# Performance work log

Hardware: AMD Instinct MI355X
Metric: run time of the kernel (lower is better)

Reference implementation:

```python
import jax, jax.numpy as jnp
import numpy as np


def setup_inputs() -> dict:
    key = jax.random.key(0)
    k1, k2, k3 = jax.random.split(key, 3)
    Lq, Lkv, H, D = 2048, 2048, 16, 128
    return {
        "query": jax.random.normal(k1, (Lq, H, D), dtype=jnp.float32),
        "key": jax.random.normal(k2, (Lkv, H, D), dtype=jnp.float32),
        "value": jax.random.normal(k3, (Lkv, H, D), dtype=jnp.float32),
    }


def reference(query, key, value):
    # query: [Lq, H, D], key: [Lkv, H, D], value: [Lkv, H, Dv]
    # Original module performs chunked online-softmax attention; the math is
    # exactly scaled-dot-product softmax attention with scale 1/sqrt(k_features).
    d = query.shape[-1]
    q = query * (1.0 / jnp.sqrt(jnp.asarray(d, dtype=query.dtype)))
    scores = jnp.einsum('qhd,khd->qhk', q, key)          # [Lq, H, Lkv]
    weights = jax.nn.softmax(scores, axis=-1)            # numerically stable online softmax equivalent
    out = jnp.einsum('qhk,khf->qhf', weights, value)     # [Lq, H, Dv]
    return out
```

## Files before the change

kernel.cpp:

```cpp
#include <hip/hip_runtime.h>
#include <hip/hip_bf16.h>

typedef __bf16 bf16x8 __attribute__((ext_vector_type(8)));
typedef __bf16 bf16x4 __attribute__((ext_vector_type(4)));
typedef __bf16 bf16x2 __attribute__((ext_vector_type(2)));
typedef float  f32x16 __attribute__((ext_vector_type(16)));
typedef float  f32x4  __attribute__((ext_vector_type(4)));

#define HD     2048
#define DH     128
#define KVT    64
#define NCH    16
#define NSPLIT 2
#define NROWS  32768
#define VSTR   68

__global__ __launch_bounds__(512, 2)
void fmha_kern(const float* __restrict__ Qg, const float* __restrict__ Kg,
               const float* __restrict__ Vg, float* __restrict__ wsO,
               float* __restrict__ wsML)
{
    __shared__ __align__(16) __bf16 klds[2][KVT * 128];
    __shared__ __align__(16) __bf16 vtlds[2][DH * VSTR];

    const int tid  = threadIdx.x;
    const int lane = tid & 63;
    const int wrp  = tid >> 6;
    const int g    = lane >> 5;
    const int l31  = lane & 31;

    const int b    = blockIdx.x;
    const int grp  = b & 31;
    const int qblk = b >> 5;
    const int h    = grp >> 1;
    const int sp   = grp & 1;
    const int t0   = sp * NCH;

    const float qscale = 1.4426950408889634f * 0.08838834764831845f;
    const int q = qblk * 256 + wrp * 32 + l31;

    bf16x8 qf[8];
    {
        const float* qrow = Qg + (size_t)q * HD + h * DH;
        #pragma unroll
        for (int j = 0; j < 8; ++j) {
            f32x4 a = *(const f32x4*)(qrow + j * 16 + 8 * g);
            f32x4 c = *(const f32x4*)(qrow + j * 16 + 8 * g + 4);
            bf16x8 f;
            f[0] = (__bf16)(a[0] * qscale); f[1] = (__bf16)(a[1] * qscale);
            f[2] = (__bf16)(a[2] * qscale); f[3] = (__bf16)(a[3] * qscale);
            f[4] = (__bf16)(c[0] * qscale); f[5] = (__bf16)(c[1] * qscale);
            f[6] = (__bf16)(c[2] * qscale); f[7] = (__bf16)(c[3] * qscale);
            qf[j] = f;
        }
    }

    const int krow = tid >> 3, kc = tid & 7;
    const int kvp  = tid & 31, vdv0 = (tid >> 5) * 8;
    const float* kbase = Kg + (size_t)h * DH;
    const float* vbase = Vg + (size_t)h * DH;

    f32x4 kreg0, kreg1, kreg2, kreg3, vreg0, vreg1, vreg2, vreg3;

    auto stage_load = [&](int t) {
        const float* kp = kbase + (size_t)(t * KVT + krow) * HD + kc * 8;
        kreg0 = *(const f32x4*)(kp);
        kreg1 = *(const f32x4*)(kp + 4);
        kreg2 = *(const f32x4*)(kp + 64);
        kreg3 = *(const f32x4*)(kp + 68);
        const float* vp = vbase + (size_t)(t * KVT + 2 * kvp) * HD + vdv0;
        vreg0 = *(const f32x4*)(vp);
        vreg1 = *(const f32x4*)(vp + 4);
        vreg2 = *(const f32x4*)(vp + HD);
        vreg3 = *(const f32x4*)(vp + HD + 4);
    };

    auto stage_write = [&](int buf) {
        bf16x8 k0, k1;
        k0[0]=(__bf16)kreg0[0]; k0[1]=(__bf16)kreg0[1]; k0[2]=(__bf16)kreg0[2]; k0[3]=(__bf16)kreg0[3];
        k0[4]=(__bf16)kreg1[0]; k0[5]=(__bf16)kreg1[1]; k0[6]=(__bf16)kreg1[2]; k0[7]=(__bf16)kreg1[3];
        k1[0]=(__bf16)kreg2[0]; k1[1]=(__bf16)kreg2[1]; k1[2]=(__bf16)kreg2[2]; k1[3]=(__bf16)kreg2[3];
        k1[4]=(__bf16)kreg3[0]; k1[5]=(__bf16)kreg3[1]; k1[6]=(__bf16)kreg3[2]; k1[7]=(__bf16)kreg3[3];
        const int swz = (krow & 7) << 3;
        *(bf16x8*)&klds[buf][krow * 128 + ((kc * 8) ^ swz)]      = k0;
        *(bf16x8*)&klds[buf][krow * 128 + ((kc * 8 + 64) ^ swz)] = k1;
        #pragma unroll
        for (int e = 0; e < 8; ++e) {
            bf16x2 w;
            w[0] = (__bf16)((e < 4) ? vreg0[e & 3] : vreg1[e & 3]);
            w[1] = (__bf16)((e < 4) ? vreg2[e & 3] : vreg3[e & 3]);
            *(bf16x2*)&vtlds[buf][(vdv0 + e) * VSTR + 2 * kvp] = w;
        }
    };

    auto block_sync = []() {
        asm volatile("s_waitcnt lgkmcnt(0)" ::: "memory");
        __builtin_amdgcn_s_barrier();
    };

    float mrun = -1e30f, lrun = 0.0f;
    f32x16 o0, o1, o2, o3;
    #pragma unroll
    for (int r = 0; r < 16; ++r) { o0[r] = 0.f; o1[r] = 0.f; o2[r] = 0.f; o3[r] = 0.f; }

    stage_load(t0);
    stage_write(0);
    stage_load(t0 + 1);
    block_sync();

    const int kswz = (l31 & 7) << 3;

    #pragma unroll 2
    for (int tt = 0; tt < NCH; ++tt) {
        const int cur = tt & 1;

        f32x16 s0, s1;
        #pragma unroll
        for (int r = 0; r < 16; ++r) { s0[r] = 0.f; s1[r] = 0.f; }
        __builtin_amdgcn_s_setprio(1);
        #pragma unroll
        for (int j = 0; j < 8; ++j) {
            bf16x8 kf0 = *(const bf16x8*)&klds[cur][l31 * 128 + ((j * 16 + 8 * g) ^ kswz)];
            s0 = __builtin_amdgcn_mfma_f32_32x32x16_bf16(kf0, qf[j], s0, 0, 0, 0);
            bf16x8 kf1 = *(const bf16x8*)&klds[cur][(32 + l31) * 128 + ((j * 16 + 8 * g) ^ kswz)];
            s1 = __builtin_amdgcn_mfma_f32_32x32x16_bf16(kf1, qf[j], s1, 0, 0, 0);
        }
        __builtin_amdgcn_s_setprio(0);

        if (tt + 1 < NCH) stage_write(cur ^ 1);
        if (tt + 2 < NCH) stage_load(t0 + tt + 2);

        float m16[8];
        #pragma unroll
        for (int r = 0; r < 8; ++r)
            m16[r] = fmaxf(fmaxf(s0[r], s0[r + 8]), fmaxf(s1[r], s1[r + 8]));
        float tmax = fmaxf(fmaxf(fmaxf(m16[0], m16[4]), fmaxf(m16[1], m16[5])),
                           fmaxf(fmaxf(m16[2], m16[6]), fmaxf(m16[3], m16[7])));
        tmax = fmaxf(tmax, __shfl_xor(tmax, 32, 64));

        if (__any(tmax > mrun + 8.0f)) {
            const float mnew  = fmaxf(mrun, tmax);
            const float alpha = __builtin_amdgcn_exp2f(mrun - mnew);
            lrun *= alpha;
            #pragma unroll
            for (int r = 0; r < 16; ++r) { o0[r] *= alpha; o1[r] *= alpha; o2[r] *= alpha; o3[r] *= alpha; }
            mrun = mnew;
        }

        float p0[16], p1[16];
        #pragma unroll
        for (int r = 0; r < 16; ++r) {
            p0[r] = __builtin_amdgcn_exp2f(s0[r] - mrun);
            p1[r] = __builtin_amdgcn_exp2f(s1[r] - mrun);
        }
        float ps = 0.f;
        #pragma unroll
        for (int r = 0; r < 16; ++r) ps += p0[r] + p1[r];
        lrun += ps;

        bf16x8 pfa0, pfa1, pfb0, pfb1;
        #pragma unroll
        for (int e = 0; e < 8; ++e) {
            pfa0[e] = (__bf16)p0[e]; pfa1[e] = (__bf16)p0[8 + e];
            pfb0[e] = (__bf16)p1[e]; pfb1[e] = (__bf16)p1[8 + e];
        }

        __builtin_amdgcn_s_setprio(1);
        #pragma unroll
        for (int bb = 0; bb < 4; ++bb) {
            const __bf16* vb = &vtlds[cur][(bb * 32 + l31) * VSTR];
            f32x16& oo = (bb == 0) ? o0 : (bb == 1) ? o1 : (bb == 2) ? o2 : o3;
            bf16x8 va;
            bf16x4 a0, a1;
            a0 = *(const bf16x4*)(vb + 4 * g);
            a1 = *(const bf16x4*)(vb + 8 + 4 * g);
            va[0]=a0[0]; va[1]=a0[1]; va[2]=a0[2]; va[3]=a0[3];
            va[4]=a1[0]; va[5]=a1[1]; va[6]=a1[2]; va[7]=a1[3];
            oo = __builtin_amdgcn_mfma_f32_32x32x16_bf16(va, pfa0, oo, 0, 0, 0);
            a0 = *(const bf16x4*)(vb + 16 + 4 * g);
            a1 = *(const bf16x4*)(vb + 24 + 4 * g);
            va[0]=a0[0]; va[1]=a0[1]; va[2]=a0[2]; va[3]=a0[3];
            va[4]=a1[0]; va[5]=a1[1]; va[6]=a1[2]; va[7]=a1[3];
            oo = __builtin_amdgcn_mfma_f32_32x32x16_bf16(va, pfa1, oo, 0, 0, 0);
            a0 = *(const bf16x4*)(vb + 32 + 4 * g);
            a1 = *(const bf16x4*)(vb + 40 + 4 * g);
            va[0]=a0[0]; va[1]=a0[1]; va[2]=a0[2]; va[3]=a0[3];
            va[4]=a1[0]; va[5]=a1[1]; va[6]=a1[2]; va[7]=a1[3];
            oo = __builtin_amdgcn_mfma_f32_32x32x16_bf16(va, pfb0, oo, 0, 0, 0);
            a0 = *(const bf16x4*)(vb + 48 + 4 * g);
            a1 = *(const bf16x4*)(vb + 56 + 4 * g);
            va[0]=a0[0]; va[1]=a0[1]; va[2]=a0[2]; va[3]=a0[3];
            va[4]=a1[0]; va[5]=a1[1]; va[6]=a1[2]; va[7]=a1[3];
            oo = __builtin_amdgcn_mfma_f32_32x32x16_bf16(va, pfb1, oo, 0, 0, 0);
        }
        __builtin_amdgcn_s_setprio(0);

        if (tt + 1 < NCH) block_sync();
    }

    const float ltot  = lrun + __shfl_xor(lrun, 32, 64);
    const int   rowid = q * 16 + h;

    float* orow = wsO + ((size_t)sp * NROWS + rowid) * 128;
    #pragma unroll
    for (int bb = 0; bb < 4; ++bb) {
        const f32x16& oo = (bb == 0) ? o0 : (bb == 1) ? o1 : (bb == 2) ? o2 : o3;
        #pragma unroll
        for (int jj = 0; jj < 4; ++jj) {
            f32x4 v;
            v[0] = oo[4*jj+0]; v[1] = oo[4*jj+1]; v[2] = oo[4*jj+2]; v[3] = oo[4*jj+3];
            *(f32x4*)(orow + bb * 32 + 8 * jj + 4 * g) = v;
        }
    }
    if (lane < 32) {
        float* ml = wsML + ((size_t)sp * NROWS + rowid) * 2;
        ml[0] = mrun;
        ml[1] = ltot;
    }
}

__global__ __launch_bounds__(256, 4)
void fmha_combine(const float* __restrict__ wsO, const float* __restrict__ wsML,
                  float* __restrict__ Og)
{
    const int tid   = threadIdx.x;
    const int rowid = blockIdx.x * 8 + (tid >> 5);
    const int c     = (tid & 31) * 4;

    float m[NSPLIT], l[NSPLIT];
    float M = -1e30f;
    #pragma unroll
    for (int s = 0; s < NSPLIT; ++s) {
        const float* ml = wsML + ((size_t)s * NROWS + rowid) * 2;
        m[s] = ml[0];
        l[s] = ml[1];
        M = fmaxf(M, m[s]);
    }
    float L = 0.f, w[NSPLIT];
    #pragma unroll
    for (int s = 0; s < NSPLIT; ++s) {
        w[s] = __builtin_amdgcn_exp2f(m[s] - M);
        L += l[s] * w[s];
    }
    const float inv = 1.0f / L;

    f32x4 acc; acc[0] = 0.f; acc[1] = 0.f; acc[2] = 0.f; acc[3] = 0.f;
    #pragma unroll
    for (int s = 0; s < NSPLIT; ++s) {
        f32x4 v = *(const f32x4*)(wsO + ((size_t)s * NROWS + rowid) * 128 + c);
        acc[0] += v[0] * w[s]; acc[1] += v[1] * w[s];
        acc[2] += v[2] * w[s]; acc[3] += v[3] * w[s];
    }
    f32x4 r;
    r[0] = acc[0] * inv; r[1] = acc[1] * inv; r[2] = acc[2] * inv; r[3] = acc[3] * inv;
    *(f32x4*)(Og + (size_t)rowid * 128 + c) = r;
}

__global__ __launch_bounds__(256, 2)
void fmha_fb(const float* __restrict__ Qg, const float* __restrict__ Kg,
             const float* __restrict__ Vg, float* __restrict__ Og)
{
    __shared__ __align__(16) __bf16 klds[2][32 * 128];
    __shared__ __align__(16) __bf16 vtlds[2][DH * 36];

    const int tid  = threadIdx.x;
    const int lane = tid & 63;
    const int wrp  = tid >> 6;
    const int g    = lane >> 5;
    const int l31  = lane & 31;

    const int b    = blockIdx.x;
    const int h    = 2 * (b & 7) + ((b >> 3) >> 4);
    const int qblk = (b >> 3) & 15;

    const float qscale = 1.4426950408889634f * 0.08838834764831845f;
    const int q = qblk * 128 + wrp * 32 + l31;

    bf16x8 qf[8];
    {
        const float* qrow = Qg + (size_t)q * HD + h * DH;
        #pragma unroll
        for (int db = 0; db < 8; ++db) {
            f32x4 a = *(const f32x4*)(qrow + db * 16 + 8 * g);
            f32x4 c = *(const f32x4*)(qrow + db * 16 + 8 * g + 4);
            bf16x8 f;
            f[0] = (__bf16)(a[0] * qscale); f[1] = (__bf16)(a[1] * qscale);
            f[2] = (__bf16)(a[2] * qscale); f[3] = (__bf16)(a[3] * qscale);
            f[4] = (__bf16)(c[0] * qscale); f[5] = (__bf16)(c[1] * qscale);
            f[6] = (__bf16)(c[2] * qscale); f[7] = (__bf16)(c[3] * qscale);
            qf[db] = f;
        }
    }

    const int krow = tid >> 3, kc = tid & 7;
    const int vkv  = tid & 31, vdv0 = (tid >> 5) * 16;
    const float* kbase = Kg + (size_t)h * DH;
    const float* vbase = Vg + (size_t)h * DH;

    f32x4 kreg0, kreg1, kreg2, kreg3, vreg0, vreg1, vreg2, vreg3;

    auto stage_load = [&](int t) {
        const float* kp = kbase + (size_t)(t * 32 + krow) * HD + kc * 8;
        kreg0 = *(const f32x4*)(kp);
        kreg1 = *(const f32x4*)(kp + 4);
        kreg2 = *(const f32x4*)(kp + 64);
        kreg3 = *(const f32x4*)(kp + 68);
        const float* vp = vbase + (size_t)(t * 32 + vkv) * HD + vdv0;
        vreg0 = *(const f32x4*)(vp);
        vreg1 = *(const f32x4*)(vp + 4);
        vreg2 = *(const f32x4*)(vp + 8);
        vreg3 = *(const f32x4*)(vp + 12);
    };

    auto stage_write = [&](int buf) {
        bf16x8 k0, k1;
        k0[0]=(__bf16)kreg0[0]; k0[1]=(__bf16)kreg0[1]; k0[2]=(__bf16)kreg0[2]; k0[3]=(__bf16)kreg0[3];
        k0[4]=(__bf16)kreg1[0]; k0[5]=(__bf16)kreg1[1]; k0[6]=(__bf16)kreg1[2]; k0[7]=(__bf16)kreg1[3];
        k1[0]=(__bf16)kreg2[0]; k1[1]=(__bf16)kreg2[1]; k1[2]=(__bf16)kreg2[2]; k1[3]=(__bf16)kreg2[3];
        k1[4]=(__bf16)kreg3[0]; k1[5]=(__bf16)kreg3[1]; k1[6]=(__bf16)kreg3[2]; k1[7]=(__bf16)kreg3[3];
        const int swz = (krow & 7) << 3;
        *(bf16x8*)&klds[buf][krow * 128 + ((kc * 8) ^ swz)]      = k0;
        *(bf16x8*)&klds[buf][krow * 128 + ((kc * 8 + 64) ^ swz)] = k1;
        #pragma unroll
        for (int jj = 0; jj < 4; ++jj) {
            f32x4 vv = (jj == 0) ? vreg0 : (jj == 1) ? vreg1 : (jj == 2) ? vreg2 : vreg3;
            #pragma unroll
            for (int e = 0; e < 4; ++e)
                vtlds[buf][(vdv0 + jj * 4 + e) * 36 + vkv] = (__bf16)vv[e];
        }
    };

    float mrun = -1e30f, lrun = 0.0f;
    f32x16 o0, o1, o2, o3;
    #pragma unroll
    for (int r = 0; r < 16; ++r) { o0[r] = 0.f; o1[r] = 0.f; o2[r] = 0.f; o3[r] = 0.f; }

    stage_load(0);
    stage_write(0);

    for (int tt = 0; tt < 64; ++tt) {
        const int cur = tt & 1;
        if (tt + 1 < 64) stage_load(tt + 1);
        __syncthreads();

        f32x16 sa, sb;
        #pragma unroll
        for (int r = 0; r < 16; ++r) { sa[r] = 0.f; sb[r] = 0.f; }
        const int kswz = (l31 & 7) << 3;
        #pragma unroll
        for (int db = 0; db < 4; ++db) {
            bf16x8 kfa = *(const bf16x8*)&klds[cur][l31 * 128 + (((2*db)   * 16 + g * 8) ^ kswz)];
            sa = __builtin_amdgcn_mfma_f32_32x32x16_bf16(kfa, qf[2*db],   sa, 0, 0, 0);
            bf16x8 kfb = *(const bf16x8*)&klds[cur][l31 * 128 + (((2*db+1) * 16 + g * 8) ^ kswz)];
            sb = __builtin_amdgcn_mfma_f32_32x32x16_bf16(kfb, qf[2*db+1], sb, 0, 0, 0);
        }
        f32x16 s;
        #pragma unroll
        for (int r = 0; r < 16; ++r) s[r] = sa[r] + sb[r];

        float m8[8];
        #pragma unroll
        for (int r = 0; r < 8; ++r) m8[r] = fmaxf(s[r], s[r + 8]);
        float tmax = fmaxf(fmaxf(fmaxf(m8[0], m8[4]), fmaxf(m8[1], m8[5])),
                           fmaxf(fmaxf(m8[2], m8[6]), fmaxf(m8[3], m8[7])));
        tmax = fmaxf(tmax, __shfl_xor(tmax, 32, 64));

        if (__any(tmax > mrun + 8.0f)) {
            const float mnew  = fmaxf(mrun, tmax);
            const float alpha = __builtin_amdgcn_exp2f(mrun - mnew);
            lrun *= alpha;
            #pragma unroll
            for (int r = 0; r < 16; ++r) { o0[r] *= alpha; o1[r] *= alpha; o2[r] *= alpha; o3[r] *= alpha; }
            mrun = mnew;
        }

        float p[16];
        #pragma unroll
        for (int r = 0; r < 16; ++r) p[r] = __builtin_amdgcn_exp2f(s[r] - mrun);
        float ps0 = 0, ps1 = 0, ps2 = 0, ps3 = 0;
        #pragma unroll
        for (int r = 0; r < 4; ++r) { ps0 += p[r]; ps1 += p[r+4]; ps2 += p[r+8]; ps3 += p[r+12]; }
        lrun += ((ps0 + ps1) + (ps2 + ps3));

        bf16x8 pf0, pf1;
        #pragma unroll
        for (int e = 0; e < 8; ++e) { pf0[e] = (__bf16)p[e]; pf1[e] = (__bf16)p[8 + e]; }

        #pragma unroll
        for (int bb = 0; bb < 4; ++bb) {
            const __bf16* vb = &vtlds[cur][(bb * 32 + l31) * 36];
            bf16x4 a0 = *(const bf16x4*)(vb + 4 * g);
            bf16x4 a1 = *(const bf16x4*)(vb + 8 + 4 * g);
            bf16x8 va;
            va[0]=a0[0]; va[1]=a0[1]; va[2]=a0[2]; va[3]=a0[3];
            va[4]=a1[0]; va[5]=a1[1]; va[6]=a1[2]; va[7]=a1[3];
            f32x16& oo = (bb == 0) ? o0 : (bb == 1) ? o1 : (bb == 2) ? o2 : o3;
            oo = __builtin_amdgcn_mfma_f32_32x32x16_bf16(va, pf0, oo, 0, 0, 0);
            bf16x4 b0 = *(const bf16x4*)(vb + 16 + 4 * g);
            bf16x4 b1 = *(const bf16x4*)(vb + 24 + 4 * g);
            va[0]=b0[0]; va[1]=b0[1]; va[2]=b0[2]; va[3]=b0[3];
            va[4]=b1[0]; va[5]=b1[1]; va[6]=b1[2]; va[7]=b1[3];
            oo = __builtin_amdgcn_mfma_f32_32x32x16_bf16(va, pf1, oo, 0, 0, 0);
        }

        if (tt + 1 < 64) stage_write(cur ^ 1);
    }

    const float ltot = lrun + __shfl_xor(lrun, 32, 64);
    const float inv  = 1.0f / ltot;
    float* orow = Og + ((size_t)q * 16 + h) * 128;
    #pragma unroll
    for (int bb = 0; bb < 4; ++bb) {
        const f32x16& oo = (bb == 0) ? o0 : (bb == 1) ? o1 : (bb == 2) ? o2 : o3;
        #pragma unroll
        for (int jj = 0; jj < 4; ++jj) {
            f32x4 v;
            v[0] = oo[4*jj+0] * inv; v[1] = oo[4*jj+1] * inv;
            v[2] = oo[4*jj+2] * inv; v[3] = oo[4*jj+3] * inv;
            *(f32x4*)(orow + bb * 32 + 8 * jj + 4 * g) = v;
        }
    }
}

extern "C" void kernel_launch(void* const* d_in, const int* in_sizes, int n_in,
                              void* d_out, int out_size, void* d_ws, size_t ws_size,
                              hipStream_t stream) {
    const float* Q = (const float*)d_in[0];
    const float* K = (const float*)d_in[1];
    const float* V = (const float*)d_in[2];
    float* O = (float*)d_out;

    const size_t needO  = (size_t)NSPLIT * NROWS * 128;
    const size_t needML = (size_t)NSPLIT * NROWS * 2;
    const size_t need_bytes = (needO + needML) * sizeof(float);

    if (ws_size >= need_bytes) {
        float* wsO  = (float*)d_ws;
        float* wsML = wsO + needO;
        hipLaunchKernelGGL(fmha_kern, dim3(256), dim3(512), 0, stream,
                           Q, K, V, wsO, wsML);
        hipLaunchKernelGGL(fmha_combine, dim3(NROWS / 8), dim3(256), 0, stream,
                           wsO, wsML, O);
    } else {
        hipLaunchKernelGGL(fmha_fb, dim3(256), dim3(256), 0, stream, Q, K, V, O);
    }
}
```

Before: 66.65 us.

## Store split partial outputs in bf16 and rework K tile load and swizzle

```diff
diff --git a/kernel.cpp b/kernel.cpp
--- a/kernel.cpp
+++ b/kernel.cpp
@@ -15,9 +15,13 @@
 #define NROWS  32768
 #define VSTR   68
 
+__device__ __forceinline__ int kkey_of(int r) {
+    return (r & 7) ^ (((r >> 3) & 3) << 1);
+}
+
 __global__ __launch_bounds__(512, 2)
 void fmha_kern(const float* __restrict__ Qg, const float* __restrict__ Kg,
-               const float* __restrict__ Vg, float* __restrict__ wsO,
+               const float* __restrict__ Vg, __bf16* __restrict__ wsOb,
                float* __restrict__ wsML)
 {
     __shared__ __align__(16) __bf16 klds[2][KVT * 128];
@@ -63,11 +67,11 @@
     f32x4 kreg0, kreg1, kreg2, kreg3, vreg0, vreg1, vreg2, vreg3;
 
     auto stage_load = [&](int t) {
-        const float* kp = kbase + (size_t)(t * KVT + krow) * HD + kc * 8;
+        const float* kp = kbase + (size_t)(t * KVT + krow) * HD + kc * 16;
         kreg0 = *(const f32x4*)(kp);
         kreg1 = *(const f32x4*)(kp + 4);
-        kreg2 = *(const f32x4*)(kp + 64);
-        kreg3 = *(const f32x4*)(kp + 68);
+        kreg2 = *(const f32x4*)(kp + 8);
+        kreg3 = *(const f32x4*)(kp + 12);
         const float* vp = vbase + (size_t)(t * KVT + 2 * kvp) * HD + vdv0;
         vreg0 = *(const f32x4*)(vp);
         vreg1 = *(const f32x4*)(vp + 4);
@@ -81,9 +85,9 @@
         k0[4]=(__bf16)kreg1[0]; k0[5]=(__bf16)kreg1[1]; k0[6]=(__bf16)kreg1[2]; k0[7]=(__bf16)kreg1[3];
         k1[0]=(__bf16)kreg2[0]; k1[1]=(__bf16)kreg2[1]; k1[2]=(__bf16)kreg2[2]; k1[3]=(__bf16)kreg2[3];
         k1[4]=(__bf16)kreg3[0]; k1[5]=(__bf16)kreg3[1]; k1[6]=(__bf16)kreg3[2]; k1[7]=(__bf16)kreg3[3];
-        const int swz = (krow & 7) << 3;
-        *(bf16x8*)&klds[buf][krow * 128 + ((kc * 8) ^ swz)]      = k0;
-        *(bf16x8*)&klds[buf][krow * 128 + ((kc * 8 + 64) ^ swz)] = k1;
+        const int key = kkey_of(krow);
+        *(bf16x8*)&klds[buf][krow * 128 + (((kc * 2)     ^ key) << 3)] = k0;
+        *(bf16x8*)&klds[buf][krow * 128 + (((kc * 2 + 1) ^ key) << 3)] = k1;
         #pragma unroll
         for (int e = 0; e < 8; ++e) {
             bf16x2 w;
@@ -108,7 +112,7 @@
     stage_load(t0 + 1);
     block_sync();
 
-    const int kswz = (l31 & 7) << 3;
+    const int kkey = kkey_of(l31);
 
     #pragma unroll 2
     for (int tt = 0; tt < NCH; ++tt) {
@@ -120,9 +124,10 @@
         __builtin_amdgcn_s_setprio(1);
         #pragma unroll
         for (int j = 0; j < 8; ++j) {
-            bf16x8 kf0 = *(const bf16x8*)&klds[cur][l31 * 128 + ((j * 16 + 8 * g) ^ kswz)];
+            const int gcol = ((2 * j + g) ^ kkey) << 3;
+            bf16x8 kf0 = *(const bf16x8*)&klds[cur][l31 * 128 + gcol];
             s0 = __builtin_amdgcn_mfma_f32_32x32x16_bf16(kf0, qf[j], s0, 0, 0, 0);
-            bf16x8 kf1 = *(const bf16x8*)&klds[cur][(32 + l31) * 128 + ((j * 16 + 8 * g) ^ kswz)];
+            bf16x8 kf1 = *(const bf16x8*)&klds[cur][(32 + l31) * 128 + gcol];
             s1 = __builtin_amdgcn_mfma_f32_32x32x16_bf16(kf1, qf[j], s1, 0, 0, 0);
         }
         __builtin_amdgcn_s_setprio(0);
@@ -143,26 +148,25 @@
             const float alpha = __builtin_amdgcn_exp2f(mrun - mnew);
             lrun *= alpha;
             #pragma unroll
-            for (int r = 0; r < 16; ++r) { o0[r] *= alpha; o1[r] *= alpha; o2[r] *= alpha; o3[r] *= alpha; }
+            for (int r = 0; r < 16; ++r) { o0[r]*=alpha; o1[r]*=alpha; o2[r]*=alpha; o3[r]*=alpha; }
             mrun = mnew;
         }
 
-        float p0[16], p1[16];
         #pragma unroll
         for (int r = 0; r < 16; ++r) {
-            p0[r] = __builtin_amdgcn_exp2f(s0[r] - mrun);
-            p1[r] = __builtin_amdgcn_exp2f(s1[r] - mrun);
+            s0[r] = __builtin_amdgcn_exp2f(s0[r] - mrun);
+            s1[r] = __builtin_amdgcn_exp2f(s1[r] - mrun);
         }
         float ps = 0.f;
         #pragma unroll
-        for (int r = 0; r < 16; ++r) ps += p0[r] + p1[r];
+        for (int r = 0; r < 16; ++r) ps += s0[r] + s1[r];
         lrun += ps;
 
         bf16x8 pfa0, pfa1, pfb0, pfb1;
         #pragma unroll
         for (int e = 0; e < 8; ++e) {
-            pfa0[e] = (__bf16)p0[e]; pfa1[e] = (__bf16)p0[8 + e];
-            pfb0[e] = (__bf16)p1[e]; pfb1[e] = (__bf16)p1[8 + e];
+            pfa0[e] = (__bf16)s0[e]; pfa1[e] = (__bf16)s0[8 + e];
+            pfb0[e] = (__bf16)s1[e]; pfb1[e] = (__bf16)s1[8 + e];
         }
 
         __builtin_amdgcn_s_setprio(1);
@@ -201,15 +205,16 @@
     const float ltot  = lrun + __shfl_xor(lrun, 32, 64);
     const int   rowid = q * 16 + h;
 
-    float* orow = wsO + ((size_t)sp * NROWS + rowid) * 128;
+    __bf16* orow = wsOb + ((size_t)sp * NROWS + rowid) * 128;
     #pragma unroll
     for (int bb = 0; bb < 4; ++bb) {
         const f32x16& oo = (bb == 0) ? o0 : (bb == 1) ? o1 : (bb == 2) ? o2 : o3;
         #pragma unroll
         for (int jj = 0; jj < 4; ++jj) {
-            f32x4 v;
-            v[0] = oo[4*jj+0]; v[1] = oo[4*jj+1]; v[2] = oo[4*jj+2]; v[3] = oo[4*jj+3];
-            *(f32x4*)(orow + bb * 32 + 8 * jj + 4 * g) = v;
+            bf16x4 v;
+            v[0] = (__bf16)oo[4*jj+0]; v[1] = (__bf16)oo[4*jj+1];
+            v[2] = (__bf16)oo[4*jj+2]; v[3] = (__bf16)oo[4*jj+3];
+            *(bf16x4*)(orow + bb * 32 + 8 * jj + 4 * g) = v;
         }
     }
     if (lane < 32) {
@@ -220,7 +225,7 @@
 }
 
 __global__ __launch_bounds__(256, 4)
-void fmha_combine(const float* __restrict__ wsO, const float* __restrict__ wsML,
+void fmha_combine(const __bf16* __restrict__ wsOb, const float* __restrict__ wsML,
                   float* __restrict__ Og)
 {
     const int tid   = threadIdx.x;
@@ -232,8 +237,7 @@
     #pragma unroll
     for (int s = 0; s < NSPLIT; ++s) {
         const float* ml = wsML + ((size_t)s * NROWS + rowid) * 2;
-        m[s] = ml[0];
-        l[s] = ml[1];
+        m[s] = ml[0]; l[s] = ml[1];
         M = fmaxf(M, m[s]);
     }
     float L = 0.f, w[NSPLIT];
@@ -244,15 +248,15 @@
     }
     const float inv = 1.0f / L;
 
-    f32x4 acc; acc[0] = 0.f; acc[1] = 0.f; acc[2] = 0.f; acc[3] = 0.f;
+    f32x4 acc; acc[0]=0.f; acc[1]=0.f; acc[2]=0.f; acc[3]=0.f;
     #pragma unroll
     for (int s = 0; s < NSPLIT; ++s) {
-        f32x4 v = *(const f32x4*)(wsO + ((size_t)s * NROWS + rowid) * 128 + c);
-        acc[0] += v[0] * w[s]; acc[1] += v[1] * w[s];
-        acc[2] += v[2] * w[s]; acc[3] += v[3] * w[s];
+        bf16x4 v = *(const bf16x4*)(wsOb + ((size_t)s * NROWS + rowid) * 128 + c);
+        acc[0] += (float)v[0] * w[s]; acc[1] += (float)v[1] * w[s];
+        acc[2] += (float)v[2] * w[s]; acc[3] += (float)v[3] * w[s];
     }
     f32x4 r;
-    r[0] = acc[0] * inv; r[1] = acc[1] * inv; r[2] = acc[2] * inv; r[3] = acc[3] * inv;
+    r[0] = acc[0]*inv; r[1] = acc[1]*inv; r[2] = acc[2]*inv; r[3] = acc[3]*inv;
     *(f32x4*)(Og + (size_t)rowid * 128 + c) = r;
 }
 
@@ -430,17 +434,17 @@
     const float* V = (const float*)d_in[2];
     float* O = (float*)d_out;
 
-    const size_t needO  = (size_t)NSPLIT * NROWS * 128;
-    const size_t needML = (size_t)NSPLIT * NROWS * 2;
-    const size_t need_bytes = (needO + needML) * sizeof(float);
+    const size_t wsOb_b = (size_t)NSPLIT * NROWS * 128 * 2;
+    const size_t wsML_b = (size_t)NSPLIT * NROWS * 2 * 4;
+    const size_t need_bytes = wsOb_b + wsML_b;
 
     if (ws_size >= need_bytes) {
-        float* wsO  = (float*)d_ws;
-        float* wsML = wsO + needO;
+        __bf16* wsOb = (__bf16*)d_ws;
+        float*  wsML = (float*)((char*)d_ws + wsOb_b);
         hipLaunchKernelGGL(fmha_kern, dim3(256), dim3(512), 0, stream,
-                           Q, K, V, wsO, wsML);
+                           Q, K, V, wsOb, wsML);
         hipLaunchKernelGGL(fmha_combine, dim3(NROWS / 8), dim3(256), 0, stream,
-                           wsO, wsML, O);
+                           wsOb, wsML, O);
     } else {
         hipLaunchKernelGGL(fmha_fb, dim3(256), dim3(256), 0, stream, Q, K, V, O);
     }
```

Result: no change. 65.82 us (-1.3%).
